# Performance work log

Measured on AMD Instinct MI355X. Metric: run time of the kernel, lower is better.

The kernel has to match this reference:

```python
import jax, jax.numpy as jnp
import numpy as np

N = 100_000      # nodes
E = 1_200_000    # edges (before self-loops)
F_IN = 128       # num_node_features
G = 256          # number of graphs in the batch
C = 10           # num_classes
NEG_SLOPE = 0.2  # PyG GATConv default


def setup_inputs() -> dict:
    key = jax.random.key(0)
    ks = jax.random.split(key, 20)
    x = jax.random.normal(ks[0], (N, F_IN), jnp.float32)
    edge_index = jax.random.randint(ks[1], (2, E), 0, N, dtype=jnp.int32)
    # sorted graph assignment covering all G graphs (no empty segments)
    batch = (jnp.arange(N, dtype=jnp.int32) * G) // N

    def lin(k, fi, fo):
        return jax.random.normal(k, (fi, fo), jnp.float32) * (1.0 / np.sqrt(fi))

    dims = [(F_IN, 16), (16, 32), (32, 64)]
    params = {}
    for i, (fi, fo) in enumerate(dims, start=1):
        params[f"W{i}"] = lin(ks[3 * i], fi, fo)
        params[f"a{i}_src"] = jax.random.normal(ks[3 * i + 1], (fo,), jnp.float32) * 0.1
        params[f"a{i}_dst"] = jax.random.normal(ks[3 * i + 2], (fo,), jnp.float32) * 0.1
        params[f"b{i}"] = jnp.zeros((fo,), jnp.float32)
    params["fc_w"] = lin(ks[15], 64, C)
    params["fc_b"] = jnp.zeros((C,), jnp.float32)
    return {"x": x, "edge_index": edge_index, "batch": batch, **params}


def _gat_layer(x, src, dst, W, a_src, a_dst, b):
    # h = Theta x; e_ij = LeakyReLU(a_src.h_j + a_dst.h_i), softmax over dst i
    h = x @ W                                     # [N, F]
    s = h @ a_src                                 # [N]
    d = h @ a_dst                                 # [N]
    logits = jax.nn.leaky_relu(s[src] + d[dst], NEG_SLOPE)   # [E+N]
    m = jax.ops.segment_max(logits, dst, num_segments=N)     # per-dst max
    ex = jnp.exp(logits - m[dst])
    denom = jax.ops.segment_sum(ex, dst, num_segments=N)
    alpha = ex / (denom[dst] + 1e-16)             # [E+N]
    out = jax.ops.segment_sum(alpha[:, None] * h[src], dst, num_segments=N)
    return out + b


def reference(x, edge_index, batch, W1, a1_src, a1_dst, b1, W2, a2_src, a2_dst, b2,
              W3, a3_src, a3_dst, b3, fc_w, fc_b):
    # add self-loops (PyG GATConv default) -> every dst segment non-empty
    loops = jnp.arange(N, dtype=edge_index.dtype)
    src = jnp.concatenate([edge_index[0], loops])
    dst = jnp.concatenate([edge_index[1], loops])

    h = jax.nn.relu(_gat_layer(x, src, dst, W1, a1_src, a1_dst, b1))
    # F.dropout(training=False) is a no-op in eval
    h = jax.nn.relu(_gat_layer(h, src, dst, W2, a2_src, a2_dst, b2))
    h = jax.nn.relu(_gat_layer(h, src, dst, W3, a3_src, a3_dst, b3))
    pooled = jax.ops.segment_max(h, batch, num_segments=G)   # global_max_pool [G, 64]
    logits = pooled @ fc_w + fc_b
    return jax.nn.log_softmax(logits, axis=1)
```

## Files before the change

kernel.cpp:

```cpp
#include <hip/hip_runtime.h>
#include <hip/hip_bf16.h>
#include <hip/hip_fp16.h>
#include <math.h>

#define NEG_SLOPE 0.2f
#define NCHUNK 1024
#define BSHIFT 9
#define BNODES 512

__device__ __forceinline__ float leaky(float x) { return x > 0.f ? x : NEG_SLOPE * x; }

__global__ void chunk_hist(const int* __restrict__ dst, int E, int Ec, int nbuck,
                           int* __restrict__ hmatT) {
    extern __shared__ int hist[];
    int c = blockIdx.x;
    for (int b = threadIdx.x; b < nbuck; b += 256) hist[b] = 0;
    __syncthreads();
    int lo = c * Ec, hi = min(E, lo + Ec);
    for (int e = lo + threadIdx.x; e < hi; e += 256) atomicAdd(&hist[dst[e] >> BSHIFT], 1);
    __syncthreads();
    for (int b = threadIdx.x; b < nbuck; b += 256) hmatT[b * NCHUNK + c] = hist[b];
}

__global__ void mat_scan(int* __restrict__ hmatT, int* __restrict__ btot) {
    __shared__ int wsum[4];
    int b = blockIdx.x;
    int t = threadIdx.x;
    int lane = t & 63, wave = t >> 6;
    int base = b * NCHUNK + t * 4;
    int a0 = hmatT[base], a1 = hmatT[base + 1], a2 = hmatT[base + 2], a3 = hmatT[base + 3];
    int ts = a0 + a1 + a2 + a3;
    int incl = ts;
#pragma unroll
    for (int o = 1; o < 64; o <<= 1) {
        int v = __shfl_up(incl, o);
        if (lane >= o) incl += v;
    }
    if (lane == 63) wsum[wave] = incl;
    __syncthreads();
    int wadd = 0;
#pragma unroll
    for (int w = 0; w < 4; w++) if (w < wave) wadd += wsum[w];
    int excl = wadd + incl - ts;
    hmatT[base] = excl;
    hmatT[base + 1] = excl + a0;
    hmatT[base + 2] = excl + a0 + a1;
    hmatT[base + 3] = excl + a0 + a1 + a2;
    if (t == 255) btot[b] = wadd + incl;
}

__global__ void base_scan(const int* __restrict__ btot, int nbuck, int* __restrict__ bbase,
                          int* __restrict__ offs, int N, int E) {
    __shared__ int tsum[256];
    int t = threadIdx.x;
    int v = (t < nbuck) ? btot[t] : 0;
    tsum[t] = v;
    __syncthreads();
    for (int o = 1; o < 256; o <<= 1) {
        int add = (t >= o) ? tsum[t - o] : 0;
        __syncthreads();
        tsum[t] += add;
        __syncthreads();
    }
    if (t <= nbuck) bbase[t] = (t == 0) ? 0 : tsum[t - 1];
    if (t == 0) offs[N] = N + E;
}

__global__ void chunk_scatter(const int* __restrict__ src, const int* __restrict__ dst,
                              int E, int Ec, int nbuck, const int* __restrict__ hmatT,
                              const int* __restrict__ bbase, int* __restrict__ bbuf) {
    extern __shared__ int cur[];
    int c = blockIdx.x;
    for (int b = threadIdx.x; b < nbuck; b += 256) cur[b] = bbase[b] + hmatT[b * NCHUNK + c];
    __syncthreads();
    int lo = c * Ec, hi = min(E, lo + Ec);
    for (int e = lo + threadIdx.x; e < hi; e += 256) {
        int d = dst[e];
        int b = d >> BSHIFT;
        int p = atomicAdd(&cur[b], 1);
        bbuf[p] = (src[e] << BSHIFT) | (d & (BNODES - 1));
    }
}

__global__ void bucket_build(const int* __restrict__ bbase, const int* __restrict__ bbuf,
                             int N, int* __restrict__ offs, int* __restrict__ csr) {
    __shared__ int hist[BNODES];
    __shared__ int offl[BNODES];
    __shared__ int cur[BNODES];
    int b = blockIdx.x;
    int t = threadIdx.x;
    hist[t] = 0;
    __syncthreads();
    int lo = bbase[b], hi = bbase[b + 1];
    for (int j = lo + t; j < hi; j += BNODES) atomicAdd(&hist[bbuf[j] & (BNODES - 1)], 1);
    __syncthreads();
    int own = hist[t];
    for (int o = 1; o < BNODES; o <<= 1) {
        int add = (t >= o) ? hist[t - o] : 0;
        __syncthreads();
        hist[t] += add;
        __syncthreads();
    }
    int excl = hist[t] - own;
    int n = (b << BSHIFT) + t;
    int off_n = n + bbase[b] + excl;
    offl[t] = off_n;
    cur[t] = 0;
    if (n < N) {
        offs[n] = off_n;
        csr[off_n] = n;
    }
    __syncthreads();
    for (int j = lo + t; j < hi; j += BNODES) {
        int v = bbuf[j];
        int ld = v & (BNODES - 1);
        int r = atomicAdd(&cur[ld], 1);
        csr[offl[ld] + 1 + r] = v >> BSHIFT;
    }
}


template <int FIN, int FOUT>
__global__ void transform(const float* __restrict__ xin, const float* __restrict__ W,
                          const float* __restrict__ asrc, const float* __restrict__ adst,
                          __half* __restrict__ h, float* __restrict__ sv, float* __restrict__ dv,
                          int N) {
    constexpr int TPN = FOUT / 4;
    constexpr int BN  = 256 / TPN;
    constexpr int PITCH = FIN + 4;
    __shared__ float xs[BN * PITCH];
    __shared__ float wl[FIN * FOUT];
    __shared__ float al[FOUT], bl[FOUT];
    for (int j = threadIdx.x; j < FIN * FOUT; j += 256) wl[j] = W[j];
    if (threadIdx.x < FOUT) { al[threadIdx.x] = asrc[threadIdx.x]; bl[threadIdx.x] = adst[threadIdx.x]; }
    int base = blockIdx.x * BN;
    constexpr int NV = BN * FIN / 4;
    const float4* xg = (const float4*)(xin + (size_t)base * FIN);
    int limv = ((N - base) * FIN) >> 2;
    for (int v = threadIdx.x; v < NV; v += 256) {
        int n = v / (FIN / 4), c = v % (FIN / 4);
        float4 val = (v < limv) ? xg[v] : make_float4(0.f, 0.f, 0.f, 0.f);
        *(float4*)&xs[n * PITCH + c * 4] = val;
    }
    __syncthreads();
    int node_l = threadIdx.x / TPN;
    int fq = (threadIdx.x % TPN) * 4;
    int node = base + node_l;
    const float* xrow = &xs[node_l * PITCH];
    float4 acc = make_float4(0.f, 0.f, 0.f, 0.f);
#pragma unroll 8
    for (int k = 0; k < FIN; k++) {
        float xv = xrow[k];
        float4 w4 = *(const float4*)&wl[k * FOUT + fq];
        acc.x += xv * w4.x; acc.y += xv * w4.y; acc.z += xv * w4.z; acc.w += xv * w4.w;
    }
    if (node < N) {
        __half2* hp = (__half2*)(h + (size_t)node * FOUT + fq);
        hp[0] = __floats2half2_rn(acc.x, acc.y);
        hp[1] = __floats2half2_rn(acc.z, acc.w);
        float sp = acc.x * al[fq] + acc.y * al[fq + 1] + acc.z * al[fq + 2] + acc.w * al[fq + 3];
        float dp = acc.x * bl[fq] + acc.y * bl[fq + 1] + acc.z * bl[fq + 2] + acc.w * bl[fq + 3];
#pragma unroll
        for (int o = TPN / 2; o > 0; o >>= 1) { sp += __shfl_xor(sp, o); dp += __shfl_xor(dp, o); }
        if (fq == 0) { sv[node] = sp; dv[node] = dp; }
    }
}


template <int F>
__global__ void gat_fused(const __half* __restrict__ h, const float* __restrict__ sv,
                          const float* __restrict__ dv, const int* __restrict__ offs,
                          const int* __restrict__ csr, const float* __restrict__ bias,
                          float* __restrict__ ew, float* __restrict__ y, int N) {
    constexpr int L = F / 4;
    constexpr int NPB = 256 / L;
    int sub = threadIdx.x / L;
    int lane = threadIdx.x % L;
    int i = blockIdx.x * NPB + sub;
    if (i >= N) return;
    int beg = offs[i], end = offs[i + 1];
    float di = dv[i];
    float m = -1e30f;
    for (int j = beg + lane; j < end; j += L) {
        float l = leaky(sv[csr[j]] + di);
        ew[j] = l;
        m = fmaxf(m, l);
    }
#pragma unroll
    for (int o = 1; o < L; o <<= 1) m = fmaxf(m, __shfl_xor(m, o));
    float s = 0.f;
    for (int j = beg + lane; j < end; j += L) {
        float e = __expf(ew[j] - m);
        ew[j] = e;
        s += e;
    }
#pragma unroll
    for (int o = 1; o < L; o <<= 1) s += __shfl_xor(s, o);
    float inv = 1.0f / s;
    float4 acc = make_float4(0.f, 0.f, 0.f, 0.f);
#pragma unroll 2
    for (int j = beg; j < end; j++) {
        int srcj = csr[j];
        float w = ew[j];
        uint2 u = *((const uint2*)(h + (size_t)srcj * F) + lane);
        float2 f0 = __half22float2(*(const __half2*)&u.x);
        float2 f1 = __half22float2(*(const __half2*)&u.y);
        acc.x += w * f0.x; acc.y += w * f0.y; acc.z += w * f1.x; acc.w += w * f1.y;
    }
    float4 b4 = ((const float4*)bias)[lane];
    float4 v;
    v.x = fmaxf(acc.x * inv + b4.x, 0.f);
    v.y = fmaxf(acc.y * inv + b4.y, 0.f);
    v.z = fmaxf(acc.z * inv + b4.z, 0.f);
    v.w = fmaxf(acc.w * inv + b4.w, 0.f);
    ((float4*)(y + (size_t)i * F))[lane] = v;
}


__global__ void pool_head(const float* __restrict__ y, const float* __restrict__ fcw,
                          const float* __restrict__ fcb, float* __restrict__ out,
                          int N, int G, int C) {
    __shared__ float red[256];
    __shared__ float pl[64];
    int g = blockIdx.x;
    long long gl = g;
    int start = (int)((gl * N + G - 1) / G);
    int end = (int)(((gl + 1) * N + G - 1) / G);
    int f = threadIdx.x & 63, w = threadIdx.x >> 6;
    float m = 0.f;
    for (int i = start + w; i < end; i += 4) m = fmaxf(m, y[(size_t)i * 64 + f]);
    red[threadIdx.x] = m;
    __syncthreads();
    if (threadIdx.x < 64) {
        pl[f] = fmaxf(fmaxf(red[f], red[64 + f]), fmaxf(red[128 + f], red[192 + f]));
    }
    __syncthreads();
    if (threadIdx.x < 64) {
        int c = threadIdx.x;
        float z = -1e30f;
        if (c < C) {
            z = fcb[c];
            for (int k = 0; k < 64; k++) z += pl[k] * fcw[k * 10 + c];
        }
        float zm = z;
#pragma unroll
        for (int o = 1; o < 16; o <<= 1) zm = fmaxf(zm, __shfl_xor(zm, o));
        float e = (c < C) ? __expf(z - zm) : 0.f;
        float se = e;
#pragma unroll
        for (int o = 1; o < 16; o <<= 1) se += __shfl_xor(se, o);
        if (c < C) out[g * C + c] = z - zm - logf(se);
    }
}


extern "C" void kernel_launch(void* const* d_in, const int* in_sizes, int n_in,
                              void* d_out, int out_size, void* d_ws, size_t ws_size,
                              hipStream_t stream) {
    const float* x    = (const float*)d_in[0];
    const int*   eidx = (const int*)d_in[1];
    const float* W1 = (const float*)d_in[3];
    const float* a1s = (const float*)d_in[4];
    const float* a1d = (const float*)d_in[5];
    const float* b1 = (const float*)d_in[6];
    const float* W2 = (const float*)d_in[7];
    const float* a2s = (const float*)d_in[8];
    const float* a2d = (const float*)d_in[9];
    const float* b2 = (const float*)d_in[10];
    const float* W3 = (const float*)d_in[11];
    const float* a3s = (const float*)d_in[12];
    const float* a3d = (const float*)d_in[13];
    const float* b3 = (const float*)d_in[14];
    const float* fcw = (const float*)d_in[15];
    const float* fcb = (const float*)d_in[16];
    float* out = (float*)d_out;

    const int N = in_sizes[2];
    const int E = in_sizes[1] / 2;
    const int C = in_sizes[16];
    const int G = out_size / C;

    const int* src = eidx;
    const int* dst = eidx + E;

    size_t off = 0;
    auto alloc = [&](size_t bytes) -> void* {
        void* p = (char*)d_ws + off;
        off += (bytes + 255) & ~(size_t)255;
        return p;
    };
    int* offs   = (int*)alloc((size_t)(N + 1) * 4);
    int* csr    = (int*)alloc((size_t)(E + N) * 4);
    float* sbuf = (float*)alloc((size_t)N * 4);
    float* dbuf = (float*)alloc((size_t)N * 4);
    float* ew   = (float*)alloc((size_t)(E + N) * 4);
    __half* hbuf = (__half*)alloc((size_t)N * 64 * 2);
    float* ybuf = (float*)alloc((size_t)N * 64 * 4);

    const int NBUCK = (N + BNODES - 1) >> BSHIFT;
    const int Ec = (E + NCHUNK - 1) / NCHUNK;
    int* hmatT = (int*)alloc((size_t)NBUCK * NCHUNK * 4);
    int* btot  = (int*)alloc((size_t)NBUCK * 4);
    int* bbase = (int*)alloc((size_t)(NBUCK + 1) * 4);
    int* bbuf  = (int*)ybuf;

    const size_t histBytes = (size_t)NBUCK * 4;

    chunk_hist<<<NCHUNK, 256, histBytes, stream>>>(dst, E, Ec, NBUCK, hmatT);
    mat_scan<<<NBUCK, 256, 0, stream>>>(hmatT, btot);
    base_scan<<<1, 256, 0, stream>>>(btot, NBUCK, bbase, offs, N, E);
    chunk_scatter<<<NCHUNK, 256, histBytes, stream>>>(src, dst, E, Ec, NBUCK, hmatT, bbase, bbuf);
    bucket_build<<<NBUCK, BNODES, 0, stream>>>(bbase, bbuf, N, offs, csr);

    transform<128, 16><<<(N + 63) / 64, 256, 0, stream>>>(x, W1, a1s, a1d, hbuf, sbuf, dbuf, N);
    gat_fused<16><<<(N + 63) / 64, 256, 0, stream>>>(hbuf, sbuf, dbuf, offs, csr, b1, ew, ybuf, N);
    transform<16, 32><<<(N + 31) / 32, 256, 0, stream>>>(ybuf, W2, a2s, a2d, hbuf, sbuf, dbuf, N);
    gat_fused<32><<<(N + 31) / 32, 256, 0, stream>>>(hbuf, sbuf, dbuf, offs, csr, b2, ew, ybuf, N);
    transform<32, 64><<<(N + 15) / 16, 256, 0, stream>>>(ybuf, W3, a3s, a3d, hbuf, sbuf, dbuf, N);
    gat_fused<64><<<(N + 15) / 16, 256, 0, stream>>>(hbuf, sbuf, dbuf, offs, csr, b3, ew, ybuf, N);

    pool_head<<<G, 256, 0, stream>>>(ybuf, fcw, fcb, out, N, G, C);
}
```

Before: 312.2 us.

## Assign one wavefront per destination node and split edges across lane groups

The fused GAT aggregation kernel now gives each destination node a full 64-lane wavefront instead of F/4 lanes. The softmax max and sum passes stride over edges 64 at a time. The weighted feature accumulation splits the node's edges across 64/L lane subgroups and then combines the partial sums with cross-lane shuffles. This exposes more parallelism per node, especially for layer 1 with only 4 lanes, which had a serial edge loop. In exchange it launches many more blocks, adds a shuffle reduction, and leaves lanes idle when degree is low (about 13 edges on average).

```diff
diff --git a/kernel.cpp b/kernel.cpp
--- a/kernel.cpp
+++ b/kernel.cpp
@@ -173,47 +173,57 @@
                           const int* __restrict__ csr, const float* __restrict__ bias,
                           float* __restrict__ ew, float* __restrict__ y, int N) {
     constexpr int L = F / 4;
-    constexpr int NPB = 256 / L;
-    int sub = threadIdx.x / L;
-    int lane = threadIdx.x % L;
-    int i = blockIdx.x * NPB + sub;
+    constexpr int EPW = 64 / L;
+    int wave = threadIdx.x >> 6;
+    int lane = threadIdx.x & 63;
+    int i = blockIdx.x * 4 + wave;
     if (i >= N) return;
     int beg = offs[i], end = offs[i + 1];
     float di = dv[i];
     float m = -1e30f;
-    for (int j = beg + lane; j < end; j += L) {
+    for (int j = beg + lane; j < end; j += 64) {
         float l = leaky(sv[csr[j]] + di);
         ew[j] = l;
         m = fmaxf(m, l);
     }
 #pragma unroll
-    for (int o = 1; o < L; o <<= 1) m = fmaxf(m, __shfl_xor(m, o));
+    for (int o = 1; o < 64; o <<= 1) m = fmaxf(m, __shfl_xor(m, o));
     float s = 0.f;
-    for (int j = beg + lane; j < end; j += L) {
+    for (int j = beg + lane; j < end; j += 64) {
         float e = __expf(ew[j] - m);
         ew[j] = e;
         s += e;
     }
 #pragma unroll
-    for (int o = 1; o < L; o <<= 1) s += __shfl_xor(s, o);
+    for (int o = 1; o < 64; o <<= 1) s += __shfl_xor(s, o);
     float inv = 1.0f / s;
+    int esub = lane / L;
+    int flane = lane % L;
     float4 acc = make_float4(0.f, 0.f, 0.f, 0.f);
-#pragma unroll 2
-    for (int j = beg; j < end; j++) {
+    for (int j = beg + esub; j < end; j += EPW) {
         int srcj = csr[j];
         float w = ew[j];
-        uint2 u = *((const uint2*)(h + (size_t)srcj * F) + lane);
+        uint2 u = *((const uint2*)(h + (size_t)srcj * F) + flane);
         float2 f0 = __half22float2(*(const __half2*)&u.x);
         float2 f1 = __half22float2(*(const __half2*)&u.y);
         acc.x += w * f0.x; acc.y += w * f0.y; acc.z += w * f1.x; acc.w += w * f1.y;
     }
-    float4 b4 = ((const float4*)bias)[lane];
-    float4 v;
-    v.x = fmaxf(acc.x * inv + b4.x, 0.f);
-    v.y = fmaxf(acc.y * inv + b4.y, 0.f);
-    v.z = fmaxf(acc.z * inv + b4.z, 0.f);
-    v.w = fmaxf(acc.w * inv + b4.w, 0.f);
-    ((float4*)(y + (size_t)i * F))[lane] = v;
+#pragma unroll
+    for (int o = L; o < 64; o <<= 1) {
+        acc.x += __shfl_xor(acc.x, o);
+        acc.y += __shfl_xor(acc.y, o);
+        acc.z += __shfl_xor(acc.z, o);
+        acc.w += __shfl_xor(acc.w, o);
+    }
+    if (lane < L) {
+        float4 b4 = ((const float4*)bias)[flane];
+        float4 v;
+        v.x = fmaxf(acc.x * inv + b4.x, 0.f);
+        v.y = fmaxf(acc.y * inv + b4.y, 0.f);
+        v.z = fmaxf(acc.z * inv + b4.z, 0.f);
+        v.w = fmaxf(acc.w * inv + b4.w, 0.f);
+        ((float4*)(y + (size_t)i * F))[flane] = v;
+    }
 }
 
 
@@ -312,12 +322,14 @@
     chunk_scatter<<<NCHUNK, 256, histBytes, stream>>>(src, dst, E, Ec, NBUCK, hmatT, bbase, bbuf);
     bucket_build<<<NBUCK, BNODES, 0, stream>>>(bbase, bbuf, N, offs, csr);
 
+    const int NODE_BLKS = (N + 3) / 4;
+
     transform<128, 16><<<(N + 63) / 64, 256, 0, stream>>>(x, W1, a1s, a1d, hbuf, sbuf, dbuf, N);
-    gat_fused<16><<<(N + 63) / 64, 256, 0, stream>>>(hbuf, sbuf, dbuf, offs, csr, b1, ew, ybuf, N);
+    gat_fused<16><<<NODE_BLKS, 256, 0, stream>>>(hbuf, sbuf, dbuf, offs, csr, b1, ew, ybuf, N);
     transform<16, 32><<<(N + 31) / 32, 256, 0, stream>>>(ybuf, W2, a2s, a2d, hbuf, sbuf, dbuf, N);
-    gat_fused<32><<<(N + 31) / 32, 256, 0, stream>>>(hbuf, sbuf, dbuf, offs, csr, b2, ew, ybuf, N);
+    gat_fused<32><<<NODE_BLKS, 256, 0, stream>>>(hbuf, sbuf, dbuf, offs, csr, b2, ew, ybuf, N);
     transform<32, 64><<<(N + 15) / 16, 256, 0, stream>>>(ybuf, W3, a3s, a3d, hbuf, sbuf, dbuf, N);
-    gat_fused<64><<<(N + 15) / 16, 256, 0, stream>>>(hbuf, sbuf, dbuf, offs, csr, b3, ew, ybuf, N);
+    gat_fused<64><<<NODE_BLKS, 256, 0, stream>>>(hbuf, sbuf, dbuf, offs, csr, b3, ew, ybuf, N);
 
     pool_head<<<G, 256, 0, stream>>>(ybuf, fcw, fcb, out, N, G, C);
 }
```

Measured after the change: 372.4 us. +19.3%, slower.

## Use online softmax and recompute edge weights instead of storing ew buffer

Applied to the files above, without the earlier changes.

Replaces the two-pass max/sum over edges, which wrote and reread a per-edge weight buffer, with a single online-softmax pass that merges (max, sum) pairs across lanes. The aggregation loop now recomputes each edge weight from sv and di, and is unrolled by 8 so the csr, sv and h gathers are issued together to give more memory-level parallelism. This removes the global ew traffic of several passes over E+N floats per layer. In exchange it does extra exp work and redundant sv gathers in every lane, and uses more registers.

```diff
diff --git a/kernel.cpp b/kernel.cpp
--- a/kernel.cpp
+++ b/kernel.cpp
@@ -171,7 +171,7 @@
 __global__ void gat_fused(const __half* __restrict__ h, const float* __restrict__ sv,
                           const float* __restrict__ dv, const int* __restrict__ offs,
                           const int* __restrict__ csr, const float* __restrict__ bias,
-                          float* __restrict__ ew, float* __restrict__ y, int N) {
+                          float* __restrict__ y, int N) {
     constexpr int L = F / 4;
     constexpr int NPB = 256 / L;
     int sub = threadIdx.x / L;
@@ -180,28 +180,45 @@
     if (i >= N) return;
     int beg = offs[i], end = offs[i + 1];
     float di = dv[i];
-    float m = -1e30f;
+    float m = -1e30f, s = 0.f;
     for (int j = beg + lane; j < end; j += L) {
         float l = leaky(sv[csr[j]] + di);
-        ew[j] = l;
-        m = fmaxf(m, l);
-    }
-#pragma unroll
-    for (int o = 1; o < L; o <<= 1) m = fmaxf(m, __shfl_xor(m, o));
-    float s = 0.f;
-    for (int j = beg + lane; j < end; j += L) {
-        float e = __expf(ew[j] - m);
-        ew[j] = e;
-        s += e;
-    }
-#pragma unroll
-    for (int o = 1; o < L; o <<= 1) s += __shfl_xor(s, o);
+        float mn = fmaxf(m, l);
+        s = s * __expf(m - mn) + __expf(l - mn);
+        m = mn;
+    }
+#pragma unroll
+    for (int o = 1; o < L; o <<= 1) {
+        float m2 = __shfl_xor(m, o), s2 = __shfl_xor(s, o);
+        float M = fmaxf(m, m2);
+        s = s * __expf(m - M) + s2 * __expf(m2 - M);
+        m = M;
+    }
     float inv = 1.0f / s;
     float4 acc = make_float4(0.f, 0.f, 0.f, 0.f);
-#pragma unroll 2
-    for (int j = beg; j < end; j++) {
+    int j = beg;
+    for (; j + 8 <= end; j += 8) {
+        int sk[8];
+#pragma unroll
+        for (int k = 0; k < 8; k++) sk[k] = csr[j + k];
+        float svk[8];
+        uint2 uk[8];
+#pragma unroll
+        for (int k = 0; k < 8; k++) {
+            svk[k] = sv[sk[k]];
+            uk[k] = *((const uint2*)(h + (size_t)sk[k] * F) + lane);
+        }
+#pragma unroll
+        for (int k = 0; k < 8; k++) {
+            float w = __expf(leaky(svk[k] + di) - m);
+            float2 f0 = __half22float2(*(const __half2*)&uk[k].x);
+            float2 f1 = __half22float2(*(const __half2*)&uk[k].y);
+            acc.x += w * f0.x; acc.y += w * f0.y; acc.z += w * f1.x; acc.w += w * f1.y;
+        }
+    }
+    for (; j < end; j++) {
         int srcj = csr[j];
-        float w = ew[j];
+        float w = __expf(leaky(sv[srcj] + di) - m);
         uint2 u = *((const uint2*)(h + (size_t)srcj * F) + lane);
         float2 f0 = __half22float2(*(const __half2*)&u.x);
         float2 f1 = __half22float2(*(const __half2*)&u.y);
@@ -293,7 +310,6 @@
     int* csr    = (int*)alloc((size_t)(E + N) * 4);
     float* sbuf = (float*)alloc((size_t)N * 4);
     float* dbuf = (float*)alloc((size_t)N * 4);
-    float* ew   = (float*)alloc((size_t)(E + N) * 4);
     __half* hbuf = (__half*)alloc((size_t)N * 64 * 2);
     float* ybuf = (float*)alloc((size_t)N * 64 * 4);
 
@@ -313,11 +329,11 @@
     bucket_build<<<NBUCK, BNODES, 0, stream>>>(bbase, bbuf, N, offs, csr);
 
     transform<128, 16><<<(N + 63) / 64, 256, 0, stream>>>(x, W1, a1s, a1d, hbuf, sbuf, dbuf, N);
-    gat_fused<16><<<(N + 63) / 64, 256, 0, stream>>>(hbuf, sbuf, dbuf, offs, csr, b1, ew, ybuf, N);
+    gat_fused<16><<<(N + 63) / 64, 256, 0, stream>>>(hbuf, sbuf, dbuf, offs, csr, b1, ybuf, N);
     transform<16, 32><<<(N + 31) / 32, 256, 0, stream>>>(ybuf, W2, a2s, a2d, hbuf, sbuf, dbuf, N);
-    gat_fused<32><<<(N + 31) / 32, 256, 0, stream>>>(hbuf, sbuf, dbuf, offs, csr, b2, ew, ybuf, N);
+    gat_fused<32><<<(N + 31) / 32, 256, 0, stream>>>(hbuf, sbuf, dbuf, offs, csr, b2, ybuf, N);
     transform<32, 64><<<(N + 15) / 16, 256, 0, stream>>>(ybuf, W3, a3s, a3d, hbuf, sbuf, dbuf, N);
-    gat_fused<64><<<(N + 15) / 16, 256, 0, stream>>>(hbuf, sbuf, dbuf, offs, csr, b3, ew, ybuf, N);
+    gat_fused<64><<<(N + 15) / 16, 256, 0, stream>>>(hbuf, sbuf, dbuf, offs, csr, b3, ybuf, N);
 
     pool_head<<<G, 256, 0, stream>>>(ybuf, fcw, fcb, out, N, G, C);
 }
```

After: 308.0 us. No clear change (-1.4%).
